# Performance work log

Measured on AMD Instinct MI355X. Metric: run time of the kernel, lower is better.

## Reference

```python
import jax, jax.numpy as jnp
import numpy as np

B, S, IN_F, OUT_F = 4, 2048, 4096, 4096
ALPHA = 0.01

def setup_inputs() -> dict:
    key = jax.random.key(0)
    k1, k2 = jax.random.split(key, 2)
    # int8-valued activations and weights (stored as int32 per harness dtype)
    x = jax.random.randint(k1, (B, S, IN_F), -127, 127, dtype=jnp.int32)
    weight = jax.random.randint(k2, (IN_F, OUT_F), -127, 127, dtype=jnp.int32)
    bias = jnp.zeros((1, OUT_F), dtype=jnp.float16)
    alpha = jnp.full((1,), ALPHA, dtype=jnp.float32)
    return {"x": x, "weight": weight, "bias": bias, "alpha": alpha}

def reference(x, weight, bias, alpha):
    # Faithful to forward's default (non-hybrid) path:
    # y = F.linear(x.float(), weight.t().float(), bias.float()) * alpha
    # F.linear(x, W^T) == x @ W, with W shape (in_features, out_features).
    x_shape = x.shape
    xf = x.reshape(-1, x_shape[-1]).astype(jnp.float32)          # [B*S, in]
    wf = weight.astype(jnp.float32)                               # [in, out]
    y = (xf @ wf + bias.astype(jnp.float32)) * alpha              # [B*S, out]
    return y.reshape(*x_shape[:-1], -1)                           # [B, S, out]
```

## Files before the change

### kernel.cpp

```cpp
#include <hip/hip_runtime.h>
#include <hip/hip_fp16.h>

using i32x4  = __attribute__((ext_vector_type(4)))  int;
using i32x16 = __attribute__((ext_vector_type(16))) int;

static constexpr int M  = 4 * 2048;
static constexpr int N  = 4096;
static constexpr int K  = 4096;
static constexpr int NT = K / 64;
static constexpr int NDT = K / 128;
static constexpr int ATILE = 256 * 64;
static constexpr int BTILE = 128 * 64;

static constexpr int PX_BLOCKS = (int)((size_t)M * K / 16 / 256);
static constexpr int PW_BLOCKS = (int)((size_t)N * K / 16 / 256);

__device__ __forceinline__ unsigned pack4(i32x4 v) {
  return (unsigned)((v.x & 255) | ((v.y & 255) << 8) | ((v.z & 255) << 16) | (v.w << 24));
}

__global__ __launch_bounds__(256) void pack_kernel(const int* __restrict__ x,
                                                   const int* __restrict__ w,
                                                   unsigned char* __restrict__ wa,
                                                   unsigned char* __restrict__ wb) {
  if (blockIdx.x < PX_BLOCKS) {
    unsigned g = blockIdx.x * 256 + threadIdx.x;
    unsigned row = g & 255;
    unsigned kg  = (g >> 8) & 3;
    unsigned kt  = (g >> 10) & 63;
    unsigned br  = g >> 16;
    const int* src = x + ((size_t)(br * 256 + row) * K + kt * 64 + kg * 16);
    i32x4 v0 = *(const i32x4*)(src + 0);
    i32x4 v1 = *(const i32x4*)(src + 4);
    i32x4 v2 = *(const i32x4*)(src + 8);
    i32x4 v3 = *(const i32x4*)(src + 12);
    i32x4 d;
    d.x = (int)pack4(v0); d.y = (int)pack4(v1); d.z = (int)pack4(v2); d.w = (int)pack4(v3);
    *(i32x4*)(wa + (size_t)g * 16) = d;
  } else {
    unsigned g = (blockIdx.x - PX_BLOCKS) * 256 + threadIdx.x;
    unsigned col = g & 127;
    unsigned kg  = (g >> 7) & 3;
    unsigned kt  = (g >> 9) & 63;
    unsigned bn  = g >> 15;
    unsigned n   = bn * 128 + col;
    unsigned k0  = kt * 64 + kg * 16;
    const int* src = w + (size_t)k0 * N + n;
    i32x4 d;
#pragma unroll
    for (int j = 0; j < 4; ++j) {
      int b0 = src[(size_t)(j * 4 + 0) * N];
      int b1 = src[(size_t)(j * 4 + 1) * N];
      int b2 = src[(size_t)(j * 4 + 2) * N];
      int b3 = src[(size_t)(j * 4 + 3) * N];
      d[j] = (b0 & 255) | ((b1 & 255) << 8) | ((b2 & 255) << 16) | (b3 << 24);
    }
    *(i32x4*)(wb + (size_t)g * 16) = d;
  }
}


__device__ __forceinline__ void gload_lds16(const void* g, void* l) {
  __builtin_amdgcn_global_load_lds((const __attribute__((address_space(1))) unsigned int*)g,
                                   (__attribute__((address_space(3))) unsigned int*)l,
                                   16, 0, 0);
}

#define FENCE()   asm volatile("" ::: "memory")
#define BARRIER() do { FENCE(); __builtin_amdgcn_s_barrier(); FENCE(); } while (0)

__global__ __launch_bounds__(512, 2) void gemm_i8(const unsigned char* __restrict__ wa,
                                                  const unsigned char* __restrict__ wb,
                                                  const __half* __restrict__ bias,
                                                  const float* __restrict__ alphaP,
                                                  float* __restrict__ out) {
  __shared__ __align__(16) unsigned char As[3][32768];

  const int tid  = threadIdx.x;
  const int lane = tid & 63;
  const int w    = tid >> 6;
  const int cw   = w & 3;
  const int cr   = cw >> 1, cc = cw & 1;
  const int l31  = lane & 31;
  const int kgl  = lane >> 5;

  const int bc = blockIdx.x;
  const int br = blockIdx.y;

  const unsigned char* ga = wa + (size_t)br * NT * ATILE;
  const unsigned char* gb = wb + (size_t)bc * NT * BTILE;

  if (w >= 4) {
    const int poff = cw * 8192;

#define STAGE(DTI) do {                                                        \
      const unsigned char* src = ga + (size_t)(DTI) * 32768 + poff + lane * 16; \
      unsigned char* dst = &As[(DTI) % 3][poff];                               \
      gload_lds16(src +    0, dst +    0);                                     \
      gload_lds16(src + 1024, dst + 1024);                                     \
      gload_lds16(src + 2048, dst + 2048);                                     \
      gload_lds16(src + 3072, dst + 3072);                                     \
      gload_lds16(src + 4096, dst + 4096);                                     \
      gload_lds16(src + 5120, dst + 5120);                                     \
      gload_lds16(src + 6144, dst + 6144);                                     \
      gload_lds16(src + 7168, dst + 7168);                                     \
    } while (0)

    STAGE(0);
    STAGE(1);
    asm volatile("s_waitcnt vmcnt(8)" ::: "memory");
    BARRIER();
    for (int dt = 0; dt < NDT; ++dt) {
      if (dt + 2 < NDT) STAGE(dt + 2);
      if (dt + 2 < NDT)      asm volatile("s_waitcnt vmcnt(8)" ::: "memory");
      else if (dt + 1 < NDT) asm volatile("s_waitcnt vmcnt(0)" ::: "memory");
      BARRIER();
    }
#undef STAGE
    return;
  }

  const int arow = cr * 128 + l31;
  const int bcol = cc * 64 + l31;

  i32x4 b[2][2][2][2];
  i32x16 acc[4][2] = {};

#define BLOADSUB(PAR, SUB, BASE) do {                                          \
    b[PAR][SUB][0][0] = *(const i32x4*)((BASE) + (kgl)     * 2048 + (bcol +  0) * 16); \
    b[PAR][SUB][0][1] = *(const i32x4*)((BASE) + (kgl)     * 2048 + (bcol + 32) * 16); \
    b[PAR][SUB][1][0] = *(const i32x4*)((BASE) + (2 + kgl) * 2048 + (bcol +  0) * 16); \
    b[PAR][SUB][1][1] = *(const i32x4*)((BASE) + (2 + kgl) * 2048 + (bcol + 32) * 16); \
  } while (0)

#define BLOAD(PAR, DT) do {                                                    \
    const unsigned char* bt = gb + (size_t)(DT) * 16384;                       \
    BLOADSUB(PAR, 0, bt);                                                      \
    BLOADSUB(PAR, 1, bt + 8192);                                               \
  } while (0)

#define CHUNK(SLOT, SUB, KC, PAR) do {                                         \
    const unsigned char* Ap = (SLOT) + (SUB) * 16384 + ((KC) * 2 + kgl) * 4096; \
    i32x4 a0 = *(const i32x4*)(Ap + (arow +  0) * 16);                         \
    i32x4 a1 = *(const i32x4*)(Ap + (arow + 32) * 16);                         \
    i32x4 a2 = *(const i32x4*)(Ap + (arow + 64) * 16);                         \
    i32x4 a3 = *(const i32x4*)(Ap + (arow + 96) * 16);                         \
    acc[0][0] = __builtin_amdgcn_mfma_i32_32x32x32_i8(a0, b[PAR][SUB][KC][0], acc[0][0], 0, 0, 0); \
    acc[0][1] = __builtin_amdgcn_mfma_i32_32x32x32_i8(a0, b[PAR][SUB][KC][1], acc[0][1], 0, 0, 0); \
    acc[1][0] = __builtin_amdgcn_mfma_i32_32x32x32_i8(a1, b[PAR][SUB][KC][0], acc[1][0], 0, 0, 0); \
    acc[1][1] = __builtin_amdgcn_mfma_i32_32x32x32_i8(a1, b[PAR][SUB][KC][1], acc[1][1], 0, 0, 0); \
    acc[2][0] = __builtin_amdgcn_mfma_i32_32x32x32_i8(a2, b[PAR][SUB][KC][0], acc[2][0], 0, 0, 0); \
    acc[2][1] = __builtin_amdgcn_mfma_i32_32x32x32_i8(a2, b[PAR][SUB][KC][1], acc[2][1], 0, 0, 0); \
    acc[3][0] = __builtin_amdgcn_mfma_i32_32x32x32_i8(a3, b[PAR][SUB][KC][0], acc[3][0], 0, 0, 0); \
    acc[3][1] = __builtin_amdgcn_mfma_i32_32x32x32_i8(a3, b[PAR][SUB][KC][1], acc[3][1], 0, 0, 0); \
  } while (0)

#define CSTEP(DT, PAR) do {                                                    \
    if ((DT) + 1 < NDT) BLOAD(PAR ^ 1, (DT) + 1);    \
    const unsigned char* slot = &As[(DT) % 3][0];                              \
    CHUNK(slot, 0, 0, PAR);                                                    \
    CHUNK(slot, 0, 1, PAR);                                                    \
    CHUNK(slot, 1, 0, PAR);                                                    \
    CHUNK(slot, 1, 1, PAR);                                                    \
    BARRIER();                                                                 \
  } while (0)

  BLOAD(0, 0);
  BARRIER();
  for (int dt = 0; dt < NDT; dt += 2) {
    CSTEP(dt, 0);
    CSTEP(dt + 1, 1);
  }

  const float alpha = *alphaP;
  const int row0 = br * 256 + cr * 128 + 4 * kgl;
  const int col0 = bc * 128 + cc * 64 + l31;
#pragma unroll
  for (int ni = 0; ni < 2; ++ni) {
    const int col = col0 + ni * 32;
    const float bf = __half2float(bias[col]);
#pragma unroll
    for (int mi = 0; mi < 4; ++mi) {
#pragma unroll
      for (int r = 0; r < 16; ++r) {
        const int row = row0 + mi * 32 + (r & 3) + 8 * (r >> 2);
        out[(size_t)row * N + col] = ((float)acc[mi][ni][r] + bf) * alpha;
      }
    }
  }
#undef CSTEP
#undef CHUNK
#undef BLOAD
#undef BLOADSUB
}

extern "C" void kernel_launch(void* const* d_in, const int* in_sizes, int n_in,
                              void* d_out, int out_size, void* d_ws, size_t ws_size,
                              hipStream_t stream) {
  const int*    x     = (const int*)d_in[0];
  const int*    wgt   = (const int*)d_in[1];
  const __half* bias  = (const __half*)d_in[2];
  const float*  alpha = (const float*)d_in[3];
  float*        out   = (float*)d_out;

  unsigned char* wa = (unsigned char*)d_ws;
  unsigned char* wb = wa + (size_t)M * K;

  pack_kernel<<<PX_BLOCKS + PW_BLOCKS, 256, 0, stream>>>(x, wgt, wa, wb);

  dim3 grid(N / 128, M / 256);
  gemm_i8<<<grid, 512, 0, stream>>>(wa, wb, bias, alpha, out);
}
```

Baseline: 227.3 us.

## Enlarge GEMM block tile to 256x256 with eight compute waves and four producers

Each block now covers a 256x256 output tile with 8 compute waves, each owning a 64x128 sub-tile, plus 4 producer waves that stream A tiles into a triple-buffered LDS ring one 64-wide k-tile at a time. B fragments are still loaded per wave straight from global memory with register double-buffering, and MFMA sections are wrapped in s_setprio to favour matrix issue. The larger tile raises A reuse across the N dimension and halves the grid. In exchange there is one block per CU, more barriers per K sweep, and more accumulator registers per wave, which may reduce latency hiding.

Result: slower. 653.2 us (+187.4%).

```diff
diff --git a/kernel.cpp b/kernel.cpp
--- a/kernel.cpp
+++ b/kernel.cpp
@@ -8,7 +8,6 @@
 static constexpr int N  = 4096;
 static constexpr int K  = 4096;
 static constexpr int NT = K / 64;
-static constexpr int NDT = K / 128;
 static constexpr int ATILE = 256 * 64;
 static constexpr int BTILE = 128 * 64;
 
@@ -69,18 +68,16 @@
 #define FENCE()   asm volatile("" ::: "memory")
 #define BARRIER() do { FENCE(); __builtin_amdgcn_s_barrier(); FENCE(); } while (0)
 
-__global__ __launch_bounds__(512, 2) void gemm_i8(const unsigned char* __restrict__ wa,
+__global__ __launch_bounds__(768, 1) void gemm_i8(const unsigned char* __restrict__ wa,
                                                   const unsigned char* __restrict__ wb,
                                                   const __half* __restrict__ bias,
                                                   const float* __restrict__ alphaP,
                                                   float* __restrict__ out) {
-  __shared__ __align__(16) unsigned char As[3][32768];
+  __shared__ __align__(16) unsigned char As[3][ATILE];
 
   const int tid  = threadIdx.x;
   const int lane = tid & 63;
   const int w    = tid >> 6;
-  const int cw   = w & 3;
-  const int cr   = cw >> 1, cc = cw & 1;
   const int l31  = lane & 31;
   const int kgl  = lane >> 5;
 
@@ -88,99 +85,95 @@
   const int br = blockIdx.y;
 
   const unsigned char* ga = wa + (size_t)br * NT * ATILE;
-  const unsigned char* gb = wb + (size_t)bc * NT * BTILE;
-
-  if (w >= 4) {
-    const int poff = cw * 8192;
-
-#define STAGE(DTI) do {                                                        \
-      const unsigned char* src = ga + (size_t)(DTI) * 32768 + poff + lane * 16; \
-      unsigned char* dst = &As[(DTI) % 3][poff];                               \
+
+  if (w >= 8) {
+    const int pw = w - 8;
+    const int poff = pw * 4096;
+
+#define STAGE(T) do {                                                          \
+      const unsigned char* src = ga + (size_t)(T) * ATILE + poff + lane * 16;  \
+      unsigned char* dst = &As[(T) % 3][poff];                                 \
       gload_lds16(src +    0, dst +    0);                                     \
       gload_lds16(src + 1024, dst + 1024);                                     \
       gload_lds16(src + 2048, dst + 2048);                                     \
       gload_lds16(src + 3072, dst + 3072);                                     \
-      gload_lds16(src + 4096, dst + 4096);                                     \
-      gload_lds16(src + 5120, dst + 5120);                                     \
-      gload_lds16(src + 6144, dst + 6144);                                     \
-      gload_lds16(src + 7168, dst + 7168);                                     \
     } while (0)
 
     STAGE(0);
     STAGE(1);
-    asm volatile("s_waitcnt vmcnt(8)" ::: "memory");
+    asm volatile("s_waitcnt vmcnt(4)" ::: "memory");
     BARRIER();
-    for (int dt = 0; dt < NDT; ++dt) {
-      if (dt + 2 < NDT) STAGE(dt + 2);
-      if (dt + 2 < NDT)      asm volatile("s_waitcnt vmcnt(8)" ::: "memory");
-      else if (dt + 1 < NDT) asm volatile("s_waitcnt vmcnt(0)" ::: "memory");
+    for (int t = 0; t < NT; ++t) {
+      if (t + 2 < NT) STAGE(t + 2);
+      if (t + 2 < NT)      asm volatile("s_waitcnt vmcnt(4)" ::: "memory");
+      else if (t + 1 < NT) asm volatile("s_waitcnt vmcnt(0)" ::: "memory");
       BARRIER();
     }
 #undef STAGE
     return;
   }
 
-  const int arow = cr * 128 + l31;
-  const int bcol = cc * 64 + l31;
-
-  i32x4 b[2][2][2][2];
-  i32x16 acc[4][2] = {};
-
-#define BLOADSUB(PAR, SUB, BASE) do {                                          \
-    b[PAR][SUB][0][0] = *(const i32x4*)((BASE) + (kgl)     * 2048 + (bcol +  0) * 16); \
-    b[PAR][SUB][0][1] = *(const i32x4*)((BASE) + (kgl)     * 2048 + (bcol + 32) * 16); \
-    b[PAR][SUB][1][0] = *(const i32x4*)((BASE) + (2 + kgl) * 2048 + (bcol +  0) * 16); \
-    b[PAR][SUB][1][1] = *(const i32x4*)((BASE) + (2 + kgl) * 2048 + (bcol + 32) * 16); \
+  const int cr = w >> 1, cc = w & 1;
+  const int arow = cr * 64 + l31;
+  const int bcl  = l31;
+
+  const unsigned char* gbw = wb + (size_t)(bc * 2 + cc) * NT * BTILE;
+
+  i32x4 b[2][2][4];
+  i32x16 acc[2][4] = {};
+
+#define BLOAD(PAR, T) do {                                                     \
+    const unsigned char* bt = gbw + (size_t)(T) * BTILE;                       \
+    b[PAR][0][0] = *(const i32x4*)(bt + (kgl)     * 2048 + (bcl +  0) * 16);   \
+    b[PAR][0][1] = *(const i32x4*)(bt + (kgl)     * 2048 + (bcl + 32) * 16);   \
+    b[PAR][0][2] = *(const i32x4*)(bt + (kgl)     * 2048 + (bcl + 64) * 16);   \
+    b[PAR][0][3] = *(const i32x4*)(bt + (kgl)     * 2048 + (bcl + 96) * 16);   \
+    b[PAR][1][0] = *(const i32x4*)(bt + (2 + kgl) * 2048 + (bcl +  0) * 16);   \
+    b[PAR][1][1] = *(const i32x4*)(bt + (2 + kgl) * 2048 + (bcl + 32) * 16);   \
+    b[PAR][1][2] = *(const i32x4*)(bt + (2 + kgl) * 2048 + (bcl + 64) * 16);   \
+    b[PAR][1][3] = *(const i32x4*)(bt + (2 + kgl) * 2048 + (bcl + 96) * 16);   \
   } while (0)
 
-#define BLOAD(PAR, DT) do {                                                    \
-    const unsigned char* bt = gb + (size_t)(DT) * 16384;                       \
-    BLOADSUB(PAR, 0, bt);                                                      \
-    BLOADSUB(PAR, 1, bt + 8192);                                               \
-  } while (0)
-
-#define CHUNK(SLOT, SUB, KC, PAR) do {                                         \
-    const unsigned char* Ap = (SLOT) + (SUB) * 16384 + ((KC) * 2 + kgl) * 4096; \
+#define CHUNK(SLOT, KC, PAR) do {                                              \
+    const unsigned char* Ap = (SLOT) + ((KC) * 2 + kgl) * 4096;                \
     i32x4 a0 = *(const i32x4*)(Ap + (arow +  0) * 16);                         \
     i32x4 a1 = *(const i32x4*)(Ap + (arow + 32) * 16);                         \
-    i32x4 a2 = *(const i32x4*)(Ap + (arow + 64) * 16);                         \
-    i32x4 a3 = *(const i32x4*)(Ap + (arow + 96) * 16);                         \
-    acc[0][0] = __builtin_amdgcn_mfma_i32_32x32x32_i8(a0, b[PAR][SUB][KC][0], acc[0][0], 0, 0, 0); \
-    acc[0][1] = __builtin_amdgcn_mfma_i32_32x32x32_i8(a0, b[PAR][SUB][KC][1], acc[0][1], 0, 0, 0); \
-    acc[1][0] = __builtin_amdgcn_mfma_i32_32x32x32_i8(a1, b[PAR][SUB][KC][0], acc[1][0], 0, 0, 0); \
-    acc[1][1] = __builtin_amdgcn_mfma_i32_32x32x32_i8(a1, b[PAR][SUB][KC][1], acc[1][1], 0, 0, 0); \
-    acc[2][0] = __builtin_amdgcn_mfma_i32_32x32x32_i8(a2, b[PAR][SUB][KC][0], acc[2][0], 0, 0, 0); \
-    acc[2][1] = __builtin_amdgcn_mfma_i32_32x32x32_i8(a2, b[PAR][SUB][KC][1], acc[2][1], 0, 0, 0); \
-    acc[3][0] = __builtin_amdgcn_mfma_i32_32x32x32_i8(a3, b[PAR][SUB][KC][0], acc[3][0], 0, 0, 0); \
-    acc[3][1] = __builtin_amdgcn_mfma_i32_32x32x32_i8(a3, b[PAR][SUB][KC][1], acc[3][1], 0, 0, 0); \
+    acc[0][0] = __builtin_amdgcn_mfma_i32_32x32x32_i8(a0, b[PAR][KC][0], acc[0][0], 0, 0, 0); \
+    acc[0][1] = __builtin_amdgcn_mfma_i32_32x32x32_i8(a0, b[PAR][KC][1], acc[0][1], 0, 0, 0); \
+    acc[0][2] = __builtin_amdgcn_mfma_i32_32x32x32_i8(a0, b[PAR][KC][2], acc[0][2], 0, 0, 0); \
+    acc[0][3] = __builtin_amdgcn_mfma_i32_32x32x32_i8(a0, b[PAR][KC][3], acc[0][3], 0, 0, 0); \
+    acc[1][0] = __builtin_amdgcn_mfma_i32_32x32x32_i8(a1, b[PAR][KC][0], acc[1][0], 0, 0, 0); \
+    acc[1][1] = __builtin_amdgcn_mfma_i32_32x32x32_i8(a1, b[PAR][KC][1], acc[1][1], 0, 0, 0); \
+    acc[1][2] = __builtin_amdgcn_mfma_i32_32x32x32_i8(a1, b[PAR][KC][2], acc[1][2], 0, 0, 0); \
+    acc[1][3] = __builtin_amdgcn_mfma_i32_32x32x32_i8(a1, b[PAR][KC][3], acc[1][3], 0, 0, 0); \
   } while (0)
 
-#define CSTEP(DT, PAR) do {                                                    \
-    if ((DT) + 1 < NDT) BLOAD(PAR ^ 1, (DT) + 1);    \
-    const unsigned char* slot = &As[(DT) % 3][0];                              \
-    CHUNK(slot, 0, 0, PAR);                                                    \
-    CHUNK(slot, 0, 1, PAR);                                                    \
-    CHUNK(slot, 1, 0, PAR);                                                    \
-    CHUNK(slot, 1, 1, PAR);                                                    \
+#define CSTEP(T, PAR) do {                                                     \
+    if ((T) + 1 < NT) BLOAD(PAR ^ 1, (T) + 1);    \
+    const unsigned char* slot = &As[(T) % 3][0];                               \
+    __builtin_amdgcn_s_setprio(1);                                             \
+    CHUNK(slot, 0, PAR);                                                       \
+    CHUNK(slot, 1, PAR);                                                       \
+    __builtin_amdgcn_s_setprio(0);                                             \
     BARRIER();                                                                 \
   } while (0)
 
   BLOAD(0, 0);
   BARRIER();
-  for (int dt = 0; dt < NDT; dt += 2) {
-    CSTEP(dt, 0);
-    CSTEP(dt + 1, 1);
+  for (int t = 0; t < NT; t += 2) {
+    CSTEP(t, 0);
+    CSTEP(t + 1, 1);
   }
 
   const float alpha = *alphaP;
-  const int row0 = br * 256 + cr * 128 + 4 * kgl;
-  const int col0 = bc * 128 + cc * 64 + l31;
-#pragma unroll
-  for (int ni = 0; ni < 2; ++ni) {
+  const int row0 = br * 256 + cr * 64 + 4 * kgl;
+  const int col0 = bc * 256 + cc * 128 + l31;
+#pragma unroll
+  for (int ni = 0; ni < 4; ++ni) {
     const int col = col0 + ni * 32;
     const float bf = __half2float(bias[col]);
 #pragma unroll
-    for (int mi = 0; mi < 4; ++mi) {
+    for (int mi = 0; mi < 2; ++mi) {
 #pragma unroll
       for (int r = 0; r < 16; ++r) {
         const int row = row0 + mi * 32 + (r & 3) + 8 * (r >> 2);
@@ -191,7 +184,6 @@
 #undef CSTEP
 #undef CHUNK
 #undef BLOAD
-#undef BLOADSUB
 }
 
 extern "C" void kernel_launch(void* const* d_in, const int* in_sizes, int n_in,
@@ -208,6 +200,6 @@
 
   pack_kernel<<<PX_BLOCKS + PW_BLOCKS, 256, 0, stream>>>(x, wgt, wa, wb);
 
-  dim3 grid(N / 128, M / 256);
-  gemm_i8<<<grid, 512, 0, stream>>>(wa, wb, bias, alpha, out);
-}
+  dim3 grid(N / 256, M / 256);
+  gemm_i8<<<grid, 768, 0, stream>>>(wa, wb, bias, alpha, out);
+}
```
